# Kernel optimization log

Hardware: AMD Instinct MI355X
Metric: run time of the kernel (lower is better)

## Reference

```python
import jax, jax.numpy as jnp
import numpy as np

NUM_PTS = 5      # num_points_per_it
MAX_IT = 25      # RANSAC iterations
TOL = 0.1        # inlier tolerance
G_PRIOR = 0.5    # bottom fraction of image assumed ground
VAX = 1          # vertical axis index


def get_AB(pts):
    """pts (..., 3) -> A (..., 3) = [non-vertical coords, 1], Bm (..., 1) = vertical coord."""
    Bm = pts[..., VAX:VAX + 1]
    cols = [pts[..., i:i + 1] for i in range(3) if i != VAX]
    A = jnp.concatenate(cols + [jnp.ones_like(Bm)], axis=-1)
    return A, Bm


def setup_inputs() -> dict:
    key = jax.random.key(0)
    k1, k2 = jax.random.split(key)
    B, H, W = 4, 384, 1280
    points = jax.random.normal(k1, (B, 3, H, W), dtype=jnp.float32)
    N = int(G_PRIOR * H) * W  # 245760 ground-candidate points per image
    T = NUM_PTS * MAX_IT      # 125 sampled indices per image
    rand_ind = jax.random.randint(k2, (B, T), 0, N, dtype=jnp.int32)
    return {"points": points, "rand_ind": rand_ind}


def reference(points, rand_ind):
    B, _, H, W = points.shape
    gH = int(G_PRIOR * H)
    N = gH * W
    # ground candidates: bottom half of image -> (B, N, 3)
    gp = points[:, :, H - gH:, :].reshape(B, 3, N).transpose(0, 2, 1)
    # gather RANSAC samples -> (B*MAX_IT, NUM_PTS, 3), b-major order (matches torch stack+reshape)
    sampled = jnp.take_along_axis(gp, rand_ind[..., None], axis=1).reshape(B * MAX_IT, NUM_PTS, 3)
    # least-squares plane fit per hypothesis: w = inv(A^T A + 1e-6) A^T b  (scalar 1e-6 added to ALL entries, faithful to torch)
    A, Bm = get_AB(sampled)
    At = jnp.swapaxes(A, 1, 2)
    ws = jnp.linalg.inv(At @ A + 1e-6) @ At @ Bm  # (B*MAX_IT, 3, 1)
    # NOTE: original code pairs ws (b-major) with points.repeat(max_it,1,1) (it-major);
    # we replicate that pairing exactly for faithfulness.
    ps = jnp.tile(gp, (MAX_IT, 1, 1))  # (MAX_IT*B, N, 3)
    Ap, Bp = get_AB(ps)
    abs_dist = jnp.abs(Ap @ ws - Bp).reshape(B, MAX_IT, N)
    # inlier voting + best hypothesis per image
    fit = (abs_dist < TOL).astype(jnp.float32).mean(axis=2)  # (B, MAX_IT)
    best = jnp.argmax(fit, axis=1)
    best_w = ws.reshape(B, MAX_IT, 3, 1)[jnp.arange(B), best]  # (B, 3, 1)
    # distance of every pixel to selected plane
    ap = points.reshape(B, 3, H * W).transpose(0, 2, 1)
    Aa, Ba = get_AB(ap)
    dist = (Aa @ best_w - Ba).transpose(0, 2, 1).reshape(B, 1, H, W)
    # forward returns detached tensors
    return jax.lax.stop_gradient(dist), jax.lax.stop_gradient(best_w)
```

## Files before the change

### kernel.cpp

```cpp
#include <hip/hip_runtime.h>
#include <hip/hip_bf16.h>


constexpr int BN      = 4;
constexpr int H       = 384;
constexpr int W       = 1280;
constexpr int HW      = H * W;
constexpr int GH      = 192;
constexpr int NPTS    = GH * W;
constexpr int MAX_IT  = 25;
constexpr int NUM_PTS = 5;
constexpr int TOTAL_P = BN * MAX_IT;

constexpr int NGRP        = 5;
constexpr int GSZ         = 5;
constexpr int CHUNKS      = 30;
constexpr int F4_PER_CHUNK = NPTS / 4 / CHUNKS;
constexpr int ITERS       = F4_PER_CHUNK / 256;
constexpr int BLOCKS_PER_B = (HW / 4) / 256;

__global__ __launch_bounds__(128) void k_fit(
        const float* __restrict__ pts, const int* __restrict__ rind,
        double* __restrict__ wsd, float* __restrict__ wsf,
        int* __restrict__ counts) {
    int t = threadIdx.x;
    if (t < TOTAL_P) counts[t] = 0;
    if (t >= TOTAL_P) return;
    int b = t / MAX_IT;
    const float* base = pts + (size_t)b * 3 * HW + (size_t)(H - GH) * W;
    double Sxx = 0, Sxz = 0, Sx = 0, Szz = 0, Sz = 0, Sxy = 0, Szy = 0, Sy = 0;
    const int* ri = rind + b * (MAX_IT * NUM_PTS) + (t % MAX_IT) * NUM_PTS;
#pragma unroll
    for (int p = 0; p < NUM_PTS; ++p) {
        int n = ri[p];
        double x = (double)base[n];
        double y = (double)base[HW + n];
        double z = (double)base[2 * HW + n];
        Sxx += x * x; Sxz += x * z; Sx += x;
        Szz += z * z; Sz += z;
        Sxy += x * y; Szy += z * y; Sy += y;
    }
    const double e = 1e-6;
    double m00 = Sxx + e, m01 = Sxz + e, m02 = Sx + e;
    double m10 = Sxz + e, m11 = Szz + e, m12 = Sz + e;
    double m20 = Sx + e,  m21 = Sz + e,  m22 = (double)NUM_PTS + e;
    double v0 = Sxy, v1 = Szy, v2 = Sy;
    double det = m00 * (m11 * m22 - m12 * m21)
               - m01 * (m10 * m22 - m12 * m20)
               + m02 * (m10 * m21 - m11 * m20);
    double inv = 1.0 / det;
    double d0 = v0  * (m11 * m22 - m12 * m21)
              - m01 * (v1  * m22 - m12 * v2 )
              + m02 * (v1  * m21 - m11 * v2 );
    double d1 = m00 * (v1  * m22 - m12 * v2 )
              - v0  * (m10 * m22 - m12 * m20)
              + m02 * (m10 * v2  - v1  * m20);
    double d2 = m00 * (m11 * v2  - v1  * m21)
              - m01 * (m10 * v2  - v1  * m20)
              + v0  * (m10 * m21 - m11 * m20);
    double w0 = d0 * inv, w1 = d1 * inv, w2 = d2 * inv;
    wsd[t * 3 + 0] = w0; wsd[t * 3 + 1] = w1; wsd[t * 3 + 2] = w2;
    wsf[t * 3 + 0] = (float)w0; wsf[t * 3 + 1] = (float)w1; wsf[t * 3 + 2] = (float)w2;
}

__global__ __launch_bounds__(256) void k_count(
        const float* __restrict__ pts, const double* __restrict__ wsd,
        int* __restrict__ counts) {
    __shared__ double swt[GSZ][3];
    __shared__ int    spid[GSZ];
    __shared__ int    sacc[GSZ];
    int grp   = blockIdx.x % NGRP;
    int pb    = (blockIdx.x / NGRP) % BN;
    int chunk = blockIdx.x / (NGRP * BN);
    int tid   = threadIdx.x;
    if (tid < GSZ) sacc[tid] = 0;
    if (tid == 0) {
        int s = 0, lo = grp * GSZ;
        for (int b = 0; b < BN; ++b) {
            int r = ((pb - b) % BN + BN) % BN;
            for (int it = r; it < MAX_IT; it += BN) {
                if (s >= lo && s < lo + GSZ) {
                    int pi = b * MAX_IT + it;
                    int j = s - lo;
                    swt[j][0] = wsd[pi * 3 + 0];
                    swt[j][1] = wsd[pi * 3 + 1];
                    swt[j][2] = wsd[pi * 3 + 2];
                    spid[j]   = pi;
                }
                ++s;
            }
        }
    }
    __syncthreads();
    double wa0 = swt[0][0], wa1 = swt[0][1], wa2 = swt[0][2];
    double wb0 = swt[1][0], wb1 = swt[1][1], wb2 = swt[1][2];
    double wc0 = swt[2][0], wc1 = swt[2][1], wc2 = swt[2][2];
    double wd0 = swt[3][0], wd1 = swt[3][1], wd2 = swt[3][2];
    double we0 = swt[4][0], we1 = swt[4][1], we2 = swt[4][2];

    const float* base = pts + (size_t)pb * 3 * HW + (size_t)(H - GH) * W;
    const float4* px = (const float4*)base;
    const float4* py = (const float4*)(base + HW);
    const float4* pz = (const float4*)(base + 2 * HW);

    int a0 = 0, a1 = 0, a2 = 0, a3 = 0, a4 = 0;
#pragma unroll
    for (int it = 0; it < ITERS; ++it) {
        int f = chunk * F4_PER_CHUNK + it * 256 + tid;
        float4 x4 = px[f], y4 = py[f], z4 = pz[f];
#pragma unroll
        for (int e = 0; e < 4; ++e) {
            double x = (double)((const float*)&x4)[e];
            double y = (double)((const float*)&y4)[e];
            double z = (double)((const float*)&z4)[e];
            double nb = -y;
            a0 += (fabs(fma(x, wa0, fma(z, wa1, wa2 + nb))) < 0.1) ? 1 : 0;
            a1 += (fabs(fma(x, wb0, fma(z, wb1, wb2 + nb))) < 0.1) ? 1 : 0;
            a2 += (fabs(fma(x, wc0, fma(z, wc1, wc2 + nb))) < 0.1) ? 1 : 0;
            a3 += (fabs(fma(x, wd0, fma(z, wd1, wd2 + nb))) < 0.1) ? 1 : 0;
            a4 += (fabs(fma(x, we0, fma(z, we1, we2 + nb))) < 0.1) ? 1 : 0;
        }
    }
    int vals[GSZ] = {a0, a1, a2, a3, a4};
#pragma unroll
    for (int j = 0; j < GSZ; ++j) {
        int v = vals[j];
        for (int off = 32; off > 0; off >>= 1) v += __shfl_down(v, off, 64);
        if ((tid & 63) == 0) atomicAdd(&sacc[j], v);
    }
    __syncthreads();
    if (tid < GSZ) atomicAdd(&counts[spid[tid]], sacc[tid]);
}

__global__ __launch_bounds__(256) void k_dist(
        const float* __restrict__ pts, const float* __restrict__ wsf,
        const int* __restrict__ counts, float* __restrict__ out) {
    __shared__ float sw[3];
    int b   = blockIdx.x / BLOCKS_PER_B;
    int blk = blockIdx.x % BLOCKS_PER_B;
    if (threadIdx.x == 0) {
        int best = 0, bc = counts[b * MAX_IT];
        for (int it = 1; it < MAX_IT; ++it) {
            int c = counts[b * MAX_IT + it];
            if (c > bc) { bc = c; best = it; }
        }
        int pi = b * MAX_IT + best;
        sw[0] = wsf[pi * 3 + 0];
        sw[1] = wsf[pi * 3 + 1];
        sw[2] = wsf[pi * 3 + 2];
        if (blk == 0) {
            out[(size_t)BN * HW + b * 3 + 0] = sw[0];
            out[(size_t)BN * HW + b * 3 + 1] = sw[1];
            out[(size_t)BN * HW + b * 3 + 2] = sw[2];
        }
    }
    __syncthreads();
    float w0 = sw[0], w1 = sw[1], w2 = sw[2];
    const float4* px = (const float4*)(pts + (size_t)b * 3 * HW);
    const float4* py = px + HW / 4;
    const float4* pz = py + HW / 4;
    int i = blk * 256 + threadIdx.x;
    float4 x = px[i], y = py[i], z = pz[i];
    float4 r;
    r.x = w0 * x.x + w1 * z.x + w2 - y.x;
    r.y = w0 * x.y + w1 * z.y + w2 - y.y;
    r.z = w0 * x.z + w1 * z.z + w2 - y.z;
    r.w = w0 * x.w + w1 * z.w + w2 - y.w;
    ((float4*)(out + (size_t)b * HW))[i] = r;
}

extern "C" void kernel_launch(void* const* d_in, const int* in_sizes, int n_in,
                              void* d_out, int out_size, void* d_ws, size_t ws_size,
                              hipStream_t stream) {
    const float* pts  = (const float*)d_in[0];
    const int*   rind = (const int*)d_in[1];
    float* out = (float*)d_out;

    double* wsd  = (double*)d_ws;
    float*  wsf  = (float*)(wsd + TOTAL_P * 3);
    int*    cnts = (int*)(wsf + TOTAL_P * 3);

    k_fit  <<<1, 128, 0, stream>>>(pts, rind, wsd, wsf, cnts);
    k_count<<<NGRP * BN * CHUNKS, 256, 0, stream>>>(pts, wsd, cnts);
    k_dist <<<BN * BLOCKS_PER_B, 256, 0, stream>>>(pts, wsf, cnts, out);
}
```

Measured before the change: 93.16 us.

## Fuse plane fitting into counting kernel and double chunk count

Removes the separate single-block fit kernel. Each counting block now recomputes the plane fits for its five hypotheses in its first five threads, and chunk 0 writes the float weights. The count buffer is zeroed with a memset, and the chunk count doubles so the grid has more, smaller blocks. This trades redundant per-block fitting work for one fewer dependent kernel launch and better parallelism.

```diff
diff --git a/kernel.cpp b/kernel.cpp
--- a/kernel.cpp
+++ b/kernel.cpp
@@ -12,60 +12,16 @@
 constexpr int NUM_PTS = 5;
 constexpr int TOTAL_P = BN * MAX_IT;
 
-constexpr int NGRP        = 5;
-constexpr int GSZ         = 5;
-constexpr int CHUNKS      = 30;
+constexpr int NGRP         = 5;
+constexpr int GSZ          = 5;
+constexpr int CHUNKS       = 60;
 constexpr int F4_PER_CHUNK = NPTS / 4 / CHUNKS;
-constexpr int ITERS       = F4_PER_CHUNK / 256;
+constexpr int ITERS        = F4_PER_CHUNK / 256;
 constexpr int BLOCKS_PER_B = (HW / 4) / 256;
 
-__global__ __launch_bounds__(128) void k_fit(
+__global__ __launch_bounds__(256) void k_count(
         const float* __restrict__ pts, const int* __restrict__ rind,
-        double* __restrict__ wsd, float* __restrict__ wsf,
-        int* __restrict__ counts) {
-    int t = threadIdx.x;
-    if (t < TOTAL_P) counts[t] = 0;
-    if (t >= TOTAL_P) return;
-    int b = t / MAX_IT;
-    const float* base = pts + (size_t)b * 3 * HW + (size_t)(H - GH) * W;
-    double Sxx = 0, Sxz = 0, Sx = 0, Szz = 0, Sz = 0, Sxy = 0, Szy = 0, Sy = 0;
-    const int* ri = rind + b * (MAX_IT * NUM_PTS) + (t % MAX_IT) * NUM_PTS;
-#pragma unroll
-    for (int p = 0; p < NUM_PTS; ++p) {
-        int n = ri[p];
-        double x = (double)base[n];
-        double y = (double)base[HW + n];
-        double z = (double)base[2 * HW + n];
-        Sxx += x * x; Sxz += x * z; Sx += x;
-        Szz += z * z; Sz += z;
-        Sxy += x * y; Szy += z * y; Sy += y;
-    }
-    const double e = 1e-6;
-    double m00 = Sxx + e, m01 = Sxz + e, m02 = Sx + e;
-    double m10 = Sxz + e, m11 = Szz + e, m12 = Sz + e;
-    double m20 = Sx + e,  m21 = Sz + e,  m22 = (double)NUM_PTS + e;
-    double v0 = Sxy, v1 = Szy, v2 = Sy;
-    double det = m00 * (m11 * m22 - m12 * m21)
-               - m01 * (m10 * m22 - m12 * m20)
-               + m02 * (m10 * m21 - m11 * m20);
-    double inv = 1.0 / det;
-    double d0 = v0  * (m11 * m22 - m12 * m21)
-              - m01 * (v1  * m22 - m12 * v2 )
-              + m02 * (v1  * m21 - m11 * v2 );
-    double d1 = m00 * (v1  * m22 - m12 * v2 )
-              - v0  * (m10 * m22 - m12 * m20)
-              + m02 * (m10 * v2  - v1  * m20);
-    double d2 = m00 * (m11 * v2  - v1  * m21)
-              - m01 * (m10 * v2  - v1  * m20)
-              + v0  * (m10 * m21 - m11 * m20);
-    double w0 = d0 * inv, w1 = d1 * inv, w2 = d2 * inv;
-    wsd[t * 3 + 0] = w0; wsd[t * 3 + 1] = w1; wsd[t * 3 + 2] = w2;
-    wsf[t * 3 + 0] = (float)w0; wsf[t * 3 + 1] = (float)w1; wsf[t * 3 + 2] = (float)w2;
-}
-
-__global__ __launch_bounds__(256) void k_count(
-        const float* __restrict__ pts, const double* __restrict__ wsd,
-        int* __restrict__ counts) {
+        float* __restrict__ wsf, int* __restrict__ counts) {
     __shared__ double swt[GSZ][3];
     __shared__ int    spid[GSZ];
     __shared__ int    sacc[GSZ];
@@ -73,22 +29,56 @@
     int pb    = (blockIdx.x / NGRP) % BN;
     int chunk = blockIdx.x / (NGRP * BN);
     int tid   = threadIdx.x;
-    if (tid < GSZ) sacc[tid] = 0;
-    if (tid == 0) {
-        int s = 0, lo = grp * GSZ;
+    if (tid < GSZ) {
+        sacc[tid] = 0;
+        int target = grp * GSZ + tid;
+        int s = 0, pi = 0;
         for (int b = 0; b < BN; ++b) {
             int r = ((pb - b) % BN + BN) % BN;
             for (int it = r; it < MAX_IT; it += BN) {
-                if (s >= lo && s < lo + GSZ) {
-                    int pi = b * MAX_IT + it;
-                    int j = s - lo;
-                    swt[j][0] = wsd[pi * 3 + 0];
-                    swt[j][1] = wsd[pi * 3 + 1];
-                    swt[j][2] = wsd[pi * 3 + 2];
-                    spid[j]   = pi;
-                }
+                if (s == target) pi = b * MAX_IT + it;
                 ++s;
             }
+        }
+        spid[tid] = pi;
+        int fb = pi / MAX_IT, fit_it = pi % MAX_IT;
+        const float* base = pts + (size_t)fb * 3 * HW + (size_t)(H - GH) * W;
+        const int* ri = rind + fb * (MAX_IT * NUM_PTS) + fit_it * NUM_PTS;
+        double Sxx = 0, Sxz = 0, Sx = 0, Szz = 0, Sz = 0, Sxy = 0, Szy = 0, Sy = 0;
+#pragma unroll
+        for (int p = 0; p < NUM_PTS; ++p) {
+            int n = ri[p];
+            double x = (double)base[n];
+            double y = (double)base[HW + n];
+            double z = (double)base[2 * HW + n];
+            Sxx += x * x; Sxz += x * z; Sx += x;
+            Szz += z * z; Sz += z;
+            Sxy += x * y; Szy += z * y; Sy += y;
+        }
+        const double e = 1e-6;
+        double m00 = Sxx + e, m01 = Sxz + e, m02 = Sx + e;
+        double m10 = Sxz + e, m11 = Szz + e, m12 = Sz + e;
+        double m20 = Sx + e,  m21 = Sz + e,  m22 = (double)NUM_PTS + e;
+        double v0 = Sxy, v1 = Szy, v2 = Sy;
+        double det = m00 * (m11 * m22 - m12 * m21)
+                   - m01 * (m10 * m22 - m12 * m20)
+                   + m02 * (m10 * m21 - m11 * m20);
+        double inv = 1.0 / det;
+        double d0 = v0  * (m11 * m22 - m12 * m21)
+                  - m01 * (v1  * m22 - m12 * v2 )
+                  + m02 * (v1  * m21 - m11 * v2 );
+        double d1 = m00 * (v1  * m22 - m12 * v2 )
+                  - v0  * (m10 * m22 - m12 * m20)
+                  + m02 * (m10 * v2  - v1  * m20);
+        double d2 = m00 * (m11 * v2  - v1  * m21)
+                  - m01 * (m10 * v2  - v1  * m20)
+                  + v0  * (m10 * m21 - m11 * m20);
+        double w0 = d0 * inv, w1 = d1 * inv, w2 = d2 * inv;
+        swt[tid][0] = w0; swt[tid][1] = w1; swt[tid][2] = w2;
+        if (chunk == 0) {
+            wsf[pi * 3 + 0] = (float)w0;
+            wsf[pi * 3 + 1] = (float)w1;
+            wsf[pi * 3 + 2] = (float)w2;
         }
     }
     __syncthreads();
@@ -176,11 +166,10 @@
     const int*   rind = (const int*)d_in[1];
     float* out = (float*)d_out;
 
-    double* wsd  = (double*)d_ws;
-    float*  wsf  = (float*)(wsd + TOTAL_P * 3);
-    int*    cnts = (int*)(wsf + TOTAL_P * 3);
+    float* wsf  = (float*)d_ws;
+    int*   cnts = (int*)(wsf + TOTAL_P * 3);
 
-    k_fit  <<<1, 128, 0, stream>>>(pts, rind, wsd, wsf, cnts);
-    k_count<<<NGRP * BN * CHUNKS, 256, 0, stream>>>(pts, wsd, cnts);
+    hipMemsetAsync(cnts, 0, TOTAL_P * sizeof(int), stream);
+    k_count<<<NGRP * BN * CHUNKS, 256, 0, stream>>>(pts, rind, wsf, cnts);
     k_dist <<<BN * BLOCKS_PER_B, 256, 0, stream>>>(pts, wsf, cnts, out);
 }
```

Measured after the change: 87.02 us. 1.07x faster.
